# Performance work log

Measured on AMD Instinct MI355X. Metric: run time of the kernel, lower is better.

## Reference

```python
import jax, jax.numpy as jnp
import numpy as np

DIM, DK, DV = 1024, 128, 128
B, S = 4, 2048

def setup_inputs() -> dict:
    key = jax.random.key(0)
    ks = jax.random.split(key, 7)
    s = lambda d: 1.0 / np.sqrt(d)
    return {
        "x":  jax.random.normal(ks[0], (B, S, DIM), dtype=jnp.float32),
        "Wq": jax.random.normal(ks[1], (DIM, DK), dtype=jnp.float32) * s(DIM),
        "bq": jax.random.normal(ks[2], (DK,), dtype=jnp.float32) * 0.02,
        "Wk": jax.random.normal(ks[3], (DIM, DK), dtype=jnp.float32) * s(DIM),
        "bk": jax.random.normal(ks[4], (DK,), dtype=jnp.float32) * 0.02,
        "Wv": jax.random.normal(ks[5], (DIM, DV), dtype=jnp.float32) * s(DIM),
        "bv": jax.random.normal(ks[6], (DV,), dtype=jnp.float32) * 0.02,
    }

def reference(x, Wq, bq, Wk, bk, Wv, bv):
    scale = DK ** (-0.5)
    q = x @ Wq + bq                      # [B,S,DK]
    k = x @ Wk + bk                      # [B,S,DK]
    v = x @ Wv + bv                      # [B,S,DV]
    attn = jnp.einsum('bsd,btd->bst', q, k) * scale  # [B,S,S]
    attn = jax.nn.softmax(attn, axis=-1)
    return jnp.einsum('bst,btd->bsd', attn, v)       # [B,S,DV]
```

## Files before the change

### kernel.cpp

```cpp
#include <hip/hip_runtime.h>

typedef unsigned short u16;
typedef unsigned int u32;
typedef __bf16 bf16;
typedef __bf16 bf16x8 __attribute__((ext_vector_type(8)));
typedef float f32x4 __attribute__((ext_vector_type(4)));
typedef u32 u32x4 __attribute__((ext_vector_type(4)));


__device__ __forceinline__ void gl_lds16(const void* g, void* l) {
  __builtin_amdgcn_global_load_lds(
      (const __attribute__((address_space(1))) void*)g,
      (__attribute__((address_space(3))) void*)l, 16, 0, 0);
}
__device__ __forceinline__ u16 bfbits(float f) {
  return __builtin_bit_cast(u16, (bf16)f);
}
__device__ __forceinline__ u32 pk2(float lo, float hi) {
  return (u32)bfbits(lo) | ((u32)bfbits(hi) << 16);
}

__global__ __launch_bounds__(256) void wprep_kernel(
    const float* __restrict__ Wq, const float* __restrict__ Wk,
    const float* __restrict__ Wv, u16* __restrict__ Wt) {
  __shared__ u16 st[64][72];
  const int tid = threadIdx.x;
  const int m = blockIdx.x >> 5, rem = blockIdx.x & 31, kt = rem >> 1, nt = rem & 1;
  const float* W = (m == 0) ? Wq : (m == 1) ? Wk : Wv;
  const int k0 = kt * 64, n0 = nt * 64;
#pragma unroll
  for (int i = 0; i < 4; ++i) {
    int kk = i * 16 + (tid >> 4), nn = (tid & 15) * 4;
    f32x4 w = *(const f32x4*)&W[(size_t)(k0 + kk) * 128 + n0 + nn];
    st[kk][nn]     = bfbits(w[0]); st[kk][nn + 1] = bfbits(w[1]);
    st[kk][nn + 2] = bfbits(w[2]); st[kk][nn + 3] = bfbits(w[3]);
  }
  __syncthreads();
#pragma unroll
  for (int i = 0; i < 4; ++i) {
    int nn = i * 16 + (tid >> 4), kk = (tid & 15) * 4;
    ushort4 u;
    u.x = st[kk][nn]; u.y = st[kk + 1][nn]; u.z = st[kk + 2][nn]; u.w = st[kk + 3][nn];
    *(ushort4*)&Wt[(size_t)m * 131072 + (size_t)(n0 + nn) * 1024 + k0 + kk] = u;
  }
}

__global__ __launch_bounds__(256) void qkv_gemm(
    const float* __restrict__ x, const u16* __restrict__ Wt,
    const float* __restrict__ bq, const float* __restrict__ bk, const float* __restrict__ bv,
    u16* __restrict__ qb, u16* __restrict__ kb, u16* __restrict__ vt)
{
  __shared__ __attribute__((aligned(16))) float sx[2][32 * 64];
  __shared__ __attribute__((aligned(16))) u16   sw[2][128 * 64];
  const int tid = threadIdx.x, wid = tid >> 6, lane = tid & 63;
  const int g = lane >> 4, q16 = lane & 15;
  const int m = blockIdx.y;
  const int row0 = blockIdx.x * 32;
  const u16* W = Wt + (size_t)m * 131072;
  const int wr = wid >> 1, wc = wid & 1;

  auto STAGE = [&](int buf, int k0) {
#pragma unroll
    for (int i = 0; i < 2; ++i) {
      int fc = i * 256 + tid; int r = fc >> 4, c = fc & 15;
      gl_lds16(x + (size_t)(row0 + r) * 1024 + k0 + ((c ^ (r & 15)) << 2),
               (char*)&sx[buf][0] + fc * 16);
    }
#pragma unroll
    for (int i = 0; i < 4; ++i) {
      int fc = i * 256 + tid; int r = fc >> 3, c = fc & 7;
      gl_lds16(W + (size_t)r * 1024 + k0 + ((c ^ (r & 7)) << 3),
               (char*)&sw[buf][0] + fc * 16);
    }
  };

  f32x4 acc[4] = {};
  STAGE(0, 0);
  asm volatile("s_waitcnt vmcnt(0)" ::: "memory");
  __syncthreads();
  int cur = 0;

  for (int kt = 0; kt < 16; ++kt) {
    if (kt < 15) STAGE(cur ^ 1, (kt + 1) * 64);
    const float* sxc = &sx[cur][0];
    const u16*   swc = &sw[cur][0];
#pragma unroll
    for (int ks = 0; ks < 2; ++ks) {
      bf16x8 af, bfr[4];
      {
        int row = wr * 16 + q16;
        int c0 = ks * 8 + g * 2;
        f32x4 lo = *(const f32x4*)(sxc + row * 64 + ((c0 ^ (row & 15)) << 2));
        f32x4 hi = *(const f32x4*)(sxc + row * 64 + (((c0 + 1) ^ (row & 15)) << 2));
        bf16x8 v;
        v[0] = (bf16)lo[0]; v[1] = (bf16)lo[1]; v[2] = (bf16)lo[2]; v[3] = (bf16)lo[3];
        v[4] = (bf16)hi[0]; v[5] = (bf16)hi[1]; v[6] = (bf16)hi[2]; v[7] = (bf16)hi[3];
        af = v;
      }
#pragma unroll
      for (int nr = 0; nr < 4; ++nr) {
        int row = wc * 64 + nr * 16 + q16;
        int ch = (ks * 4 + g) ^ (row & 7);
        bfr[nr] = *(const bf16x8*)(swc + row * 64 + ch * 8);
      }
#pragma unroll
      for (int nr = 0; nr < 4; ++nr)
        acc[nr] = __builtin_amdgcn_mfma_f32_16x16x32_bf16(af, bfr[nr], acc[nr], 0, 0, 0);
    }
    if (kt < 15) {
      asm volatile("s_waitcnt vmcnt(0)" ::: "memory");
      __syncthreads();
      cur ^= 1;
    }
  }

  const float* bias = (m == 0) ? bq : (m == 1) ? bk : bv;
  u16* qk = (m == 0) ? qb : kb;
#pragma unroll
  for (int nr = 0; nr < 4; ++nr) {
    int col = wc * 64 + nr * 16 + q16;
    float bc = bias[col];
    int grow = row0 + wr * 16 + g * 4;
    if (m == 2) {
      int bb = grow >> 11;
      int sbase = ((grow & 2047) & ~31) | (g * 8 + wr * 4);
      ushort4 u;
      u.x = bfbits(acc[nr][0] + bc);
      u.y = bfbits(acc[nr][1] + bc);
      u.z = bfbits(acc[nr][2] + bc);
      u.w = bfbits(acc[nr][3] + bc);
      *(ushort4*)&vt[(size_t)bb * 262144 + (size_t)col * 2048 + sbase] = u;
    } else {
#pragma unroll
      for (int r = 0; r < 4; ++r)
        qk[(size_t)(grow + r) * 128 + col] = bfbits(acc[nr][r] + bc);
    }
  }
}

union ALDS {
  u16 stg[4][8192];
  struct {
    float oc[4][32 * 132];
    float ml[4][2][32];
    float wfin[4][32];
  } cb;
};

__global__ __launch_bounds__(256) void attn_kernel(
    const u16* __restrict__ qb, const u16* __restrict__ kb, const u16* __restrict__ vt,
    float* __restrict__ out)
{
  __shared__ __attribute__((aligned(16))) ALDS lds;
  const int tid = threadIdx.x, wid = tid >> 6, lane = tid & 63;
  const int g = lane >> 4, q16 = lane & 15;
  const int qt = blockIdx.x, b = blockIdx.y;
  const size_t qgA = (size_t)b * 2048 + qt * 32;
  const u16* kbw = kb + ((size_t)b * 2048 + wid * 512) * 128;
  const u16* vbw = vt + (size_t)b * 262144 + wid * 512;
  u16* skw = &lds.stg[wid][0];
  u16* svw = &lds.stg[wid][4096];
  const float scale = 0.08838834764831845f;

  bf16x8 qfA[4], qfB[4];
#pragma unroll
  for (int kg = 0; kg < 4; ++kg) {
    qfA[kg] = *(const bf16x8*)&qb[(qgA + q16) * 128 + kg * 32 + g * 8];
    qfB[kg] = *(const bf16x8*)&qb[(qgA + 16 + q16) * 128 + kg * 32 + g * 8];
  }

  auto SK = [&](int t) {
#pragma unroll
    for (int i = 0; i < 8; ++i) {
      int fc = i * 64 + lane; int r = fc >> 4, c = fc & 15;
      gl_lds16(kbw + (size_t)(t * 32 + r) * 128 + ((c ^ (r & 7)) << 3),
               (char*)skw + fc * 16);
    }
  };
  auto SV = [&](int t) {
#pragma unroll
    for (int i = 0; i < 8; ++i) {
      int fc = i * 64 + lane; int r = fc >> 2, c = fc & 3;
      int h = (r ^ (r >> 2)) & 3;
      gl_lds16(vbw + (size_t)r * 2048 + t * 32 + ((c ^ h) << 3),
               (char*)svw + fc * 16);
    }
  };

  float mA = -INFINITY, lA = 0.f, mB = -INFINITY, lB = 0.f;
  f32x4 accA[8] = {}, accB[8] = {};

  SK(0); SV(0);
  for (int t = 0; t < 16; ++t) {
    asm volatile("s_waitcnt vmcnt(8)" ::: "memory");

    f32x4 sTa[2] = {}, sTb[2] = {};
#pragma unroll
    for (int kg = 0; kg < 4; ++kg)
#pragma unroll
      for (int jg = 0; jg < 2; ++jg) {
        int row = jg * 16 + q16;
        int ch = (kg * 4 + g) ^ (row & 7);
        bf16x8 kf = *(const bf16x8*)(skw + row * 128 + ch * 8);
        sTa[jg] = __builtin_amdgcn_mfma_f32_16x16x32_bf16(kf, qfA[kg], sTa[jg], 0, 0, 0);
        sTb[jg] = __builtin_amdgcn_mfma_f32_16x16x32_bf16(kf, qfB[kg], sTb[jg], 0, 0, 0);
      }
    __builtin_amdgcn_sched_barrier(0);
    if (t < 15) SK(t + 1);

    u32 WpA[2][2], WpB[2][2];
    {
      float mx = fmaxf(fmaxf(fmaxf(sTa[0][0], sTa[0][1]), fmaxf(sTa[0][2], sTa[0][3])),
                       fmaxf(fmaxf(sTa[1][0], sTa[1][1]), fmaxf(sTa[1][2], sTa[1][3])));
      mx = fmaxf(mx, __shfl_xor(mx, 16));
      mx = fmaxf(mx, __shfl_xor(mx, 32));
      float mxs = mx * scale;
      bool defer = __all(mxs <= mA + 4.0f);
      float mn = defer ? mA : fmaxf(mA, mxs);
      float rs = 0.f;
#pragma unroll
      for (int jg = 0; jg < 2; ++jg) {
        float e0 = __expf(fmaf(sTa[jg][0], scale, -mn));
        float e1 = __expf(fmaf(sTa[jg][1], scale, -mn));
        float e2 = __expf(fmaf(sTa[jg][2], scale, -mn));
        float e3 = __expf(fmaf(sTa[jg][3], scale, -mn));
        rs += (e0 + e1) + (e2 + e3);
        WpA[jg][0] = pk2(e0, e1);
        WpA[jg][1] = pk2(e2, e3);
      }
      rs += __shfl_xor(rs, 16);
      rs += __shfl_xor(rs, 32);
      if (defer) {
        lA += rs;
      } else {
        float aa = __expf(mA - mn);
        lA = lA * aa + rs; mA = mn;
#pragma unroll
        for (int dg = 0; dg < 8; ++dg) accA[dg] *= aa;
      }
    }
    {
      float mx = fmaxf(fmaxf(fmaxf(sTb[0][0], sTb[0][1]), fmaxf(sTb[0][2], sTb[0][3])),
                       fmaxf(fmaxf(sTb[1][0], sTb[1][1]), fmaxf(sTb[1][2], sTb[1][3])));
      mx = fmaxf(mx, __shfl_xor(mx, 16));
      mx = fmaxf(mx, __shfl_xor(mx, 32));
      float mxs = mx * scale;
      bool defer = __all(mxs <= mB + 4.0f);
      float mn = defer ? mB : fmaxf(mB, mxs);
      float rs = 0.f;
#pragma unroll
      for (int jg = 0; jg < 2; ++jg) {
        float e0 = __expf(fmaf(sTb[jg][0], scale, -mn));
        float e1 = __expf(fmaf(sTb[jg][1], scale, -mn));
        float e2 = __expf(fmaf(sTb[jg][2], scale, -mn));
        float e3 = __expf(fmaf(sTb[jg][3], scale, -mn));
        rs += (e0 + e1) + (e2 + e3);
        WpB[jg][0] = pk2(e0, e1);
        WpB[jg][1] = pk2(e2, e3);
      }
      rs += __shfl_xor(rs, 16);
      rs += __shfl_xor(rs, 32);
      if (defer) {
        lB += rs;
      } else {
        float aa = __expf(mB - mn);
        lB = lB * aa + rs; mB = mn;
#pragma unroll
        for (int dg = 0; dg < 8; ++dg) accB[dg] *= aa;
      }
    }

    u32x4 wa = {WpA[0][0], WpA[0][1], WpA[1][0], WpA[1][1]};
    u32x4 wb = {WpB[0][0], WpB[0][1], WpB[1][0], WpB[1][1]};
    bf16x8 pA = __builtin_bit_cast(bf16x8, wa);
    bf16x8 pB = __builtin_bit_cast(bf16x8, wb);

    if (t < 15) { asm volatile("s_waitcnt vmcnt(8)" ::: "memory"); }
    else        { asm volatile("s_waitcnt vmcnt(0)" ::: "memory"); }

#pragma unroll
    for (int dg = 0; dg < 8; ++dg) {
      int row = dg * 16 + q16;
      int ch = g ^ ((row ^ (row >> 2)) & 3);
      bf16x8 vf = *(const bf16x8*)(svw + row * 32 + ch * 8);
      accA[dg] = __builtin_amdgcn_mfma_f32_16x16x32_bf16(vf, pA, accA[dg], 0, 0, 0);
      accB[dg] = __builtin_amdgcn_mfma_f32_16x16x32_bf16(vf, pB, accB[dg], 0, 0, 0);
    }
    __builtin_amdgcn_sched_barrier(0);
    if (t < 15) SV(t + 1);
  }

  __syncthreads();
  {
    float* ocp = &lds.cb.oc[wid][0];
#pragma unroll
    for (int dg = 0; dg < 8; ++dg) {
      *(f32x4*)&ocp[q16 * 132 + dg * 16 + g * 4] = accA[dg];
      *(f32x4*)&ocp[(16 + q16) * 132 + dg * 16 + g * 4] = accB[dg];
    }
    if (g == 0) {
      lds.cb.ml[wid][0][q16] = mA; lds.cb.ml[wid][1][q16] = lA;
      lds.cb.ml[wid][0][16 + q16] = mB; lds.cb.ml[wid][1][16 + q16] = lB;
    }
  }
  __syncthreads();
  if (tid < 32) {
    int q = tid;
    float m0 = lds.cb.ml[0][0][q], m1 = lds.cb.ml[1][0][q];
    float m2 = lds.cb.ml[2][0][q], m3 = lds.cb.ml[3][0][q];
    float ms = fmaxf(fmaxf(m0, m1), fmaxf(m2, m3));
    float w0 = __expf(m0 - ms), w1 = __expf(m1 - ms);
    float w2 = __expf(m2 - ms), w3 = __expf(m3 - ms);
    float den = w0 * lds.cb.ml[0][1][q] + w1 * lds.cb.ml[1][1][q]
              + w2 * lds.cb.ml[2][1][q] + w3 * lds.cb.ml[3][1][q];
    float inv = 1.0f / den;
    lds.cb.wfin[0][q] = w0 * inv; lds.cb.wfin[1][q] = w1 * inv;
    lds.cb.wfin[2][q] = w2 * inv; lds.cb.wfin[3][q] = w3 * inv;
  }
  __syncthreads();
#pragma unroll
  for (int h = 0; h < 4; ++h) {
    int idx = h * 256 + tid;
    int q = idx >> 5, d4 = idx & 31;
    f32x4 v = lds.cb.wfin[0][q] * *(const f32x4*)&lds.cb.oc[0][q * 132 + d4 * 4]
            + lds.cb.wfin[1][q] * *(const f32x4*)&lds.cb.oc[1][q * 132 + d4 * 4]
            + lds.cb.wfin[2][q] * *(const f32x4*)&lds.cb.oc[2][q * 132 + d4 * 4]
            + lds.cb.wfin[3][q] * *(const f32x4*)&lds.cb.oc[3][q * 132 + d4 * 4];
    *(f32x4*)&out[((size_t)b * 2048 + qt * 32 + q) * 128 + d4 * 4] = v;
  }
}

extern "C" void kernel_launch(void* const* d_in, const int* in_sizes, int n_in,
                              void* d_out, int out_size, void* d_ws, size_t ws_size,
                              hipStream_t stream)
{
  (void)in_sizes; (void)n_in; (void)out_size; (void)ws_size;
  const float* x  = (const float*)d_in[0];
  const float* Wq = (const float*)d_in[1];
  const float* bq = (const float*)d_in[2];
  const float* Wk = (const float*)d_in[3];
  const float* bk = (const float*)d_in[4];
  const float* Wv = (const float*)d_in[5];
  const float* bv = (const float*)d_in[6];
  char* ws = (char*)d_ws;
  u16* qbuf  = (u16*)(ws);
  u16* kbuf  = (u16*)(ws + (2u << 20));
  u16* vtbuf = (u16*)(ws + (4u << 20));
  u16* Wt    = (u16*)(ws + (6u << 20));

  wprep_kernel<<<96, 256, 0, stream>>>(Wq, Wk, Wv, Wt);
  qkv_gemm<<<dim3(256, 3), 256, 0, stream>>>(x, Wt, bq, bk, bv, qbuf, kbuf, vtbuf);
  attn_kernel<<<dim3(64, 4), 256, 0, stream>>>(qbuf, kbuf, vtbuf, (float*)d_out);
}
```

Measured before the change: 56.60 us.

## Drop LDS staging in QKV GEMM and load operands directly into registers

The QKV projection GEMM no longer stages x and W tiles into double-buffered LDS with async global-to-LDS copies and barriers. Each wave now loads its MFMA fragments straight from global memory. The block tile grows to 64 rows, and each wave computes a 2x4 grid of 16x16 MFMA tiles, halving the grid. This removes LDS traffic and block-wide syncs and should let more blocks run at once. In exchange there is no explicit prefetch, so load latency must be hidden by occupancy and the caches, and W fragments are re-read from L1/L2 by every wave.

```diff
diff --git a/kernel.cpp b/kernel.cpp
--- a/kernel.cpp
+++ b/kernel.cpp
@@ -50,90 +50,71 @@
     const float* __restrict__ bq, const float* __restrict__ bk, const float* __restrict__ bv,
     u16* __restrict__ qb, u16* __restrict__ kb, u16* __restrict__ vt)
 {
-  __shared__ __attribute__((aligned(16))) float sx[2][32 * 64];
-  __shared__ __attribute__((aligned(16))) u16   sw[2][128 * 64];
   const int tid = threadIdx.x, wid = tid >> 6, lane = tid & 63;
   const int g = lane >> 4, q16 = lane & 15;
   const int m = blockIdx.y;
-  const int row0 = blockIdx.x * 32;
-  const u16* W = Wt + (size_t)m * 131072;
+  const int row0 = blockIdx.x * 64;
   const int wr = wid >> 1, wc = wid & 1;
 
-  auto STAGE = [&](int buf, int k0) {
-#pragma unroll
-    for (int i = 0; i < 2; ++i) {
-      int fc = i * 256 + tid; int r = fc >> 4, c = fc & 15;
-      gl_lds16(x + (size_t)(row0 + r) * 1024 + k0 + ((c ^ (r & 15)) << 2),
-               (char*)&sx[buf][0] + fc * 16);
-    }
-#pragma unroll
-    for (int i = 0; i < 4; ++i) {
-      int fc = i * 256 + tid; int r = fc >> 3, c = fc & 7;
-      gl_lds16(W + (size_t)r * 1024 + k0 + ((c ^ (r & 7)) << 3),
-               (char*)&sw[buf][0] + fc * 16);
-    }
-  };
-
-  f32x4 acc[4] = {};
-  STAGE(0, 0);
-  asm volatile("s_waitcnt vmcnt(0)" ::: "memory");
-  __syncthreads();
-  int cur = 0;
-
+  const float* xp[2];
+#pragma unroll
+  for (int mr = 0; mr < 2; ++mr)
+    xp[mr] = x + (size_t)(row0 + wr * 32 + mr * 16 + q16) * 1024 + g * 8;
+  const u16* wp[4];
+#pragma unroll
+  for (int nr = 0; nr < 4; ++nr)
+    wp[nr] = Wt + (size_t)m * 131072 + (size_t)(wc * 64 + nr * 16 + q16) * 1024 + g * 8;
+
+  f32x4 acc[2][4] = {};
   for (int kt = 0; kt < 16; ++kt) {
-    if (kt < 15) STAGE(cur ^ 1, (kt + 1) * 64);
-    const float* sxc = &sx[cur][0];
-    const u16*   swc = &sw[cur][0];
+    const int k0 = kt * 64;
 #pragma unroll
     for (int ks = 0; ks < 2; ++ks) {
-      bf16x8 af, bfr[4];
-      {
-        int row = wr * 16 + q16;
-        int c0 = ks * 8 + g * 2;
-        f32x4 lo = *(const f32x4*)(sxc + row * 64 + ((c0 ^ (row & 15)) << 2));
-        f32x4 hi = *(const f32x4*)(sxc + row * 64 + (((c0 + 1) ^ (row & 15)) << 2));
+      const int ko = k0 + ks * 32;
+      bf16x8 af[2], bfr[4];
+#pragma unroll
+      for (int mr = 0; mr < 2; ++mr) {
+        f32x4 lo = *(const f32x4*)(xp[mr] + ko);
+        f32x4 hi = *(const f32x4*)(xp[mr] + ko + 4);
         bf16x8 v;
         v[0] = (bf16)lo[0]; v[1] = (bf16)lo[1]; v[2] = (bf16)lo[2]; v[3] = (bf16)lo[3];
         v[4] = (bf16)hi[0]; v[5] = (bf16)hi[1]; v[6] = (bf16)hi[2]; v[7] = (bf16)hi[3];
-        af = v;
-      }
-#pragma unroll
-      for (int nr = 0; nr < 4; ++nr) {
-        int row = wc * 64 + nr * 16 + q16;
-        int ch = (ks * 4 + g) ^ (row & 7);
-        bfr[nr] = *(const bf16x8*)(swc + row * 64 + ch * 8);
+        af[mr] = v;
       }
 #pragma unroll
       for (int nr = 0; nr < 4; ++nr)
-        acc[nr] = __builtin_amdgcn_mfma_f32_16x16x32_bf16(af, bfr[nr], acc[nr], 0, 0, 0);
-    }
-    if (kt < 15) {
-      asm volatile("s_waitcnt vmcnt(0)" ::: "memory");
-      __syncthreads();
-      cur ^= 1;
+        bfr[nr] = *(const bf16x8*)(wp[nr] + ko);
+#pragma unroll
+      for (int mr = 0; mr < 2; ++mr)
+#pragma unroll
+        for (int nr = 0; nr < 4; ++nr)
+          acc[mr][nr] = __builtin_amdgcn_mfma_f32_16x16x32_bf16(af[mr], bfr[nr], acc[mr][nr], 0, 0, 0);
     }
   }
 
   const float* bias = (m == 0) ? bq : (m == 1) ? bk : bv;
   u16* qk = (m == 0) ? qb : kb;
 #pragma unroll
-  for (int nr = 0; nr < 4; ++nr) {
-    int col = wc * 64 + nr * 16 + q16;
-    float bc = bias[col];
-    int grow = row0 + wr * 16 + g * 4;
-    if (m == 2) {
-      int bb = grow >> 11;
-      int sbase = ((grow & 2047) & ~31) | (g * 8 + wr * 4);
-      ushort4 u;
-      u.x = bfbits(acc[nr][0] + bc);
-      u.y = bfbits(acc[nr][1] + bc);
-      u.z = bfbits(acc[nr][2] + bc);
-      u.w = bfbits(acc[nr][3] + bc);
-      *(ushort4*)&vt[(size_t)bb * 262144 + (size_t)col * 2048 + sbase] = u;
-    } else {
-#pragma unroll
-      for (int r = 0; r < 4; ++r)
-        qk[(size_t)(grow + r) * 128 + col] = bfbits(acc[nr][r] + bc);
+  for (int mr = 0; mr < 2; ++mr) {
+#pragma unroll
+    for (int nr = 0; nr < 4; ++nr) {
+      int col = wc * 64 + nr * 16 + q16;
+      float bc = bias[col];
+      int grow = row0 + wr * 32 + mr * 16 + g * 4;
+      if (m == 2) {
+        int bb = grow >> 11;
+        int sbase = ((grow & 2047) & ~31) | (g * 8 + mr * 4);
+        ushort4 u;
+        u.x = bfbits(acc[mr][nr][0] + bc);
+        u.y = bfbits(acc[mr][nr][1] + bc);
+        u.z = bfbits(acc[mr][nr][2] + bc);
+        u.w = bfbits(acc[mr][nr][3] + bc);
+        *(ushort4*)&vt[(size_t)bb * 262144 + (size_t)col * 2048 + sbase] = u;
+      } else {
+#pragma unroll
+        for (int r = 0; r < 4; ++r)
+          qk[(size_t)(grow + r) * 128 + col] = bfbits(acc[mr][nr][r] + bc);
+      }
     }
   }
 }
@@ -349,6 +330,6 @@
   u16* Wt    = (u16*)(ws + (6u << 20));
 
   wprep_kernel<<<96, 256, 0, stream>>>(Wq, Wk, Wv, Wt);
-  qkv_gemm<<<dim3(256, 3), 256, 0, stream>>>(x, Wt, bq, bk, bv, qbuf, kbuf, vtbuf);
+  qkv_gemm<<<dim3(128, 3), 256, 0, stream>>>(x, Wt, bq, bk, bv, qbuf, kbuf, vtbuf);
   attn_kernel<<<dim3(64, 4), 256, 0, stream>>>(qbuf, kbuf, vtbuf, (float*)d_out);
 }
```

Result: slower. 98.05 us (+73.2%).
